# Optimization experiments

Hardware: AMD Instinct MI355X
Metric: run time of the kernel (lower is better)

Reference implementation:

```python
import jax, jax.numpy as jnp
import numpy as np

B, P, N, E = 4, 4, 4096, 512
QKV_DIM, HEADS = 512, 8
DH = QKV_DIM // HEADS
EPS = 1e-12  # F.normalize default eps


def setup_inputs() -> dict:
    key = jax.random.key(0)
    ks = jax.random.split(key, 5)
    s = 1.0 / np.sqrt(E)
    return {
        "x": jax.random.normal(ks[0], (B, P, N, E), dtype=jnp.float32),
        "w_qkv": jax.random.normal(ks[1], (3 * QKV_DIM, E), dtype=jnp.float32) * s,
        "b_qkv": jax.random.normal(ks[2], (3 * QKV_DIM,), dtype=jnp.float32) * 0.01,
        "temperature": jnp.ones((HEADS, 1, 1), dtype=jnp.float32),
        "w_out": jax.random.normal(ks[3], (E, QKV_DIM), dtype=jnp.float32) * (1.0 / np.sqrt(QKV_DIM)),
        "b_out": jax.random.normal(ks[4], (E,), dtype=jnp.float32) * 0.01,
    }


def _l2norm(t):
    # F.normalize(t, dim=-1): t / max(||t||_2, eps)
    n = jnp.sqrt(jnp.sum(t * t, axis=-1, keepdims=True))
    return t / jnp.maximum(n, EPS)


def reference(x, w_qkv, b_qkv, temperature, w_out, b_out):
    b, p, n, _ = x.shape
    qkv = x @ w_qkv.T + b_qkv                      # (b,p,n,3*qkv)
    q, k, v = jnp.split(qkv, 3, axis=-1)
    def to_heads(t):
        # (b,p,n,h*dh) -> (b,p,h,dh,n)  (channels-as-tokens)
        t = t.reshape(b, p, n, HEADS, DH)
        return jnp.transpose(t, (0, 1, 3, 4, 2))
    q, k, v = to_heads(q), to_heads(k), to_heads(v)
    q = _l2norm(q)                                  # normalize over tokens n
    k = _l2norm(k)
    # channel-wise (dh x dh) attention per head, temperature-scaled
    attn = jnp.einsum('bphdn,bphen->bphde', q, k) * temperature  # (b,p,h,dh,dh)
    attn = jax.nn.softmax(attn, axis=-1)
    out = jnp.einsum('bphde,bphen->bphdn', attn, v)               # (b,p,h,dh,n)
    # torch rearrange 'b p h n d -> b p d (h n)' on (b,p,h,dh,n) -> (b,p,n,h*dh)
    out = jnp.transpose(out, (0, 1, 4, 2, 3)).reshape(b, p, n, HEADS * DH)
    return out @ w_out.T + b_out
```

## Files before the change

### kernel.cpp

```cpp
#include <hip/hip_runtime.h>
#include <stdint.h>

typedef unsigned short u16;
typedef __bf16 bf16x8 __attribute__((ext_vector_type(8)));
typedef float f32x4 __attribute__((ext_vector_type(4)));

#define AS1 __attribute__((address_space(1)))
#define AS3 __attribute__((address_space(3)))

__device__ __forceinline__ void gload_lds16(u16* lds_wave_base, const u16* g) {
  __builtin_amdgcn_global_load_lds((AS1 void*)g, (AS3 void*)lds_wave_base, 16, 0, 0);
}

__device__ __forceinline__ u16 f2bf(float f) {
  unsigned int u = __float_as_uint(f);
  u += 0x7fffu + ((u >> 16) & 1u);
  return (u16)(u >> 16);
}

__global__ void cast_f32_bf16(const float* __restrict__ in, u16* __restrict__ out, int n8) {
  int i = blockIdx.x * blockDim.x + threadIdx.x;
  if (i >= n8) return;
  const float4* p = (const float4*)in + (size_t)i * 2;
  float4 a = p[0], b = p[1];
  uint2 lo, hi;
  lo.x = (unsigned)f2bf(a.x) | ((unsigned)f2bf(a.y) << 16);
  lo.y = (unsigned)f2bf(a.z) | ((unsigned)f2bf(a.w) << 16);
  hi.x = (unsigned)f2bf(b.x) | ((unsigned)f2bf(b.y) << 16);
  hi.y = (unsigned)f2bf(b.z) | ((unsigned)f2bf(b.w) << 16);
  uint2* o = (uint2*)out + (size_t)i * 2;
  o[0] = lo;
  o[1] = hi;
}

template <int MODE>
__global__ __launch_bounds__(256) void gemm_bt(const u16* __restrict__ gA,
                                               const u16* __restrict__ gB,
                                               const float* __restrict__ bias,
                                               void* __restrict__ gC,
                                               float* __restrict__ ssq) {
  constexpr int SMEM_U16 = (MODE == 2) ? 8192 : (128 * 136);
  __shared__ __align__(16) u16 smem[SMEM_U16];
  u16* As = smem;
  u16* Bs = smem + 4096;
  const int t = threadIdx.x;
  const int w = t >> 6, l = t & 63;
  const int lrow = l & 15, quad = l >> 4;
  const int wm = (w >> 1) * 64, wn = (w & 1) * 64;
  const int m0 = (MODE == 0 ? blockIdx.y : blockIdx.x) * 128;
  const int n0 = (MODE == 0 ? blockIdx.x : blockIdx.y) * 128;
  const u16* pA = gA;
  const u16* pB = gB;
  if (MODE == 2) {
    pA += (size_t)blockIdx.z * (512 * 512);
    pB += (size_t)blockIdx.z * (4096 * 512);
  }
  const int srow = w * 32 + (l >> 2);
  const int scol = (l & 3) * 8;
  const u16* ga0 = pA + (size_t)(m0 + srow) * 512 + scol;
  const u16* ga1 = pA + (size_t)(m0 + srow + 16) * 512 + scol;
  const u16* gb0 = pB + (size_t)(n0 + srow) * 512 + scol;
  const u16* gb1 = pB + (size_t)(n0 + srow + 16) * 512 + scol;
  u16* lA0 = &As[w * 1024];
  u16* lA1 = &As[w * 1024 + 512];
  u16* lB0 = &Bs[w * 1024];
  u16* lB1 = &Bs[w * 1024 + 512];

  f32x4 acc[4][4];
#pragma unroll
  for (int mi = 0; mi < 4; ++mi)
#pragma unroll
    for (int ni = 0; ni < 4; ++ni) acc[mi][ni] = (f32x4){0.f, 0.f, 0.f, 0.f};

#pragma unroll 1
  for (int k0 = 0; k0 < 512; k0 += 32) {
    gload_lds16(lA0, ga0 + k0);
    gload_lds16(lA1, ga1 + k0);
    gload_lds16(lB0, gb0 + k0);
    gload_lds16(lB1, gb1 + k0);
    __syncthreads();
    bf16x8 af[4], bfr[4];
#pragma unroll
    for (int mi = 0; mi < 4; ++mi)
      af[mi] = *(const bf16x8*)&As[(wm + mi * 16 + lrow) * 32 + quad * 8];
#pragma unroll
    for (int ni = 0; ni < 4; ++ni)
      bfr[ni] = *(const bf16x8*)&Bs[(wn + ni * 16 + lrow) * 32 + quad * 8];
#pragma unroll
    for (int mi = 0; mi < 4; ++mi)
#pragma unroll
      for (int ni = 0; ni < 4; ++ni)
        acc[mi][ni] = __builtin_amdgcn_mfma_f32_16x16x32_bf16(af[mi], bfr[ni], acc[mi][ni], 0, 0, 0);
    __syncthreads();
  }

  if (MODE == 2) {
#pragma unroll
    for (int mi = 0; mi < 4; ++mi) {
      const int mrow = m0 + wm + mi * 16 + quad * 4;
      const float4 bb = *(const float4*)&bias[mrow];
#pragma unroll
      for (int ni = 0; ni < 4; ++ni) {
        const int ncol = n0 + wn + ni * 16 + lrow;
        f32x4 v = acc[mi][ni];
        float4 o;
        o.x = v[0] + bb.x;
        o.y = v[1] + bb.y;
        o.z = v[2] + bb.z;
        o.w = v[3] + bb.w;
        *(float4*)((float*)gC + (((size_t)blockIdx.z * 4096 + ncol) * 512 + mrow)) = o;
      }
    }
  } else {
    float ss[4] = {0.f, 0.f, 0.f, 0.f};
#pragma unroll
    for (int mi = 0; mi < 4; ++mi) {
      const int mrow_l = wm + mi * 16 + quad * 4;
#pragma unroll
      for (int ni = 0; ni < 4; ++ni) {
        const int ncol_l = wn + ni * 16 + lrow;
        f32x4 v = acc[mi][ni];
        float f0, f1, f2, f3;
        if (MODE == 0) {
          const float bb = bias[n0 + ncol_l];
          f0 = v[0] + bb;
          f1 = v[1] + bb;
          f2 = v[2] + bb;
          f3 = v[3] + bb;
          ss[ni] += f0 * f0 + f1 * f1 + f2 * f2 + f3 * f3;
        } else {
          const float4 bb = *(const float4*)&bias[1024 + m0 + mrow_l];
          f0 = v[0] + bb.x;
          f1 = v[1] + bb.y;
          f2 = v[2] + bb.z;
          f3 = v[3] + bb.w;
        }
        uint2 pk;
        pk.x = (unsigned)f2bf(f0) | ((unsigned)f2bf(f1) << 16);
        pk.y = (unsigned)f2bf(f2) | ((unsigned)f2bf(f3) << 16);
        *(uint2*)&smem[ncol_l * 136 + mrow_l] = pk;
      }
    }
    if (MODE == 0) {
#pragma unroll
      for (int ni = 0; ni < 4; ++ni) {
        float s = ss[ni];
        s += __shfl_xor(s, 16);
        s += __shfl_xor(s, 32);
        if (quad == 0)
          atomicAdd(&ssq[((m0 >> 12) << 10) + n0 + wn + ni * 16 + lrow], s);
      }
    }
    __syncthreads();
    u16* outp = (u16*)gC;
#pragma unroll
    for (int j = 0; j < 8; ++j) {
      const int g = j * 256 + t;
      const int r = g >> 4;
      const int c = (g & 15) * 8;
      uint4 val = *(const uint4*)&smem[r * 136 + c];
      size_t gaddr;
      if (MODE == 0) {
        gaddr = ((size_t)(m0 >> 12) << 22) + ((size_t)(n0 + r) << 12) + (size_t)((m0 & 4095) + c);
      } else {
        const int tokg = n0 + r;
        gaddr = (size_t)(tokg >> 12) * (4096 * 512) + (size_t)(tokg & 4095) * 512 + (size_t)(m0 + c);
      }
      *(uint4*)(outp + gaddr) = val;
    }
  }
}

__global__ __launch_bounds__(512) void attn_weff(const u16* __restrict__ QKt,
                                                 const u16* __restrict__ wout,
                                                 const float* __restrict__ temperature,
                                                 const float* __restrict__ ssq,
                                                 u16* __restrict__ Weff) {
  __shared__ __align__(16) float sattn[64 * 64];
  __shared__ __align__(16) u16 sattnT[64 * 64];
  __shared__ float rn[128];
  const int blk = blockIdx.x;
  const int bp = blk >> 3, h = blk & 7;
  const int t = threadIdx.x, w = t >> 6, l = t & 63;
  const int lrow = l & 15, quad = l >> 4;
  const u16* base = QKt + ((size_t)bp << 22);

  for (int i = t; i < 4096; i += 512) sattn[i] = 0.f;

  if (t < 128) {
    const int ch = (t < 64) ? (h * 64 + t) : (448 + h * 64 + t);
    const float nn = sqrtf(ssq[(bp << 10) + ch]);
    rn[t] = 1.f / fmaxf(nn, 1e-12f);
  }

  f32x4 acc[4][4];
#pragma unroll
  for (int mi = 0; mi < 4; ++mi)
#pragma unroll
    for (int ni = 0; ni < 4; ++ni) acc[mi][ni] = (f32x4){0.f, 0.f, 0.f, 0.f};
  const u16* qb = base + ((size_t)(h * 64) << 12);
  const u16* kb = base + ((size_t)(512 + h * 64) << 12);
  const int nbase = w * 512;
#pragma unroll 1
  for (int ks = 0; ks < 16; ++ks) {
    const int nn = nbase + ks * 32 + quad * 8;
    bf16x8 af[4], bfr[4];
#pragma unroll
    for (int mi = 0; mi < 4; ++mi)
      af[mi] = *(const bf16x8*)(qb + (((size_t)(mi * 16 + lrow)) << 12) + nn);
#pragma unroll
    for (int ni = 0; ni < 4; ++ni)
      bfr[ni] = *(const bf16x8*)(kb + (((size_t)(ni * 16 + lrow)) << 12) + nn);
#pragma unroll
    for (int mi = 0; mi < 4; ++mi)
#pragma unroll
      for (int ni = 0; ni < 4; ++ni)
        acc[mi][ni] = __builtin_amdgcn_mfma_f32_16x16x32_bf16(af[mi], bfr[ni], acc[mi][ni], 0, 0, 0);
  }
  __syncthreads();
  for (int ww = 0; ww < 8; ++ww) {
    if (w == ww) {
#pragma unroll
      for (int mi = 0; mi < 4; ++mi)
#pragma unroll
        for (int ni = 0; ni < 4; ++ni)
#pragma unroll
          for (int r = 0; r < 4; ++r)
            sattn[(mi * 16 + quad * 4 + r) * 64 + ni * 16 + lrow] += acc[mi][ni][r];
    }
    __syncthreads();
  }

  if (t < 64) {
    const int d = t;
    const float rq = rn[d];
    const float tmp = temperature[h];
    float mx = -1e30f;
    for (int e = 0; e < 64; ++e) {
      const int idx = (e + d) & 63;
      float v = sattn[d * 64 + idx] * rq * rn[64 + idx] * tmp;
      sattn[d * 64 + idx] = v;
      mx = fmaxf(mx, v);
    }
    float s = 0.f;
    for (int e = 0; e < 64; ++e) {
      const int idx = (e + d) & 63;
      float p = __expf(sattn[d * 64 + idx] - mx);
      s += p;
      sattn[d * 64 + idx] = p;
    }
    const float inv = 1.f / s;
    for (int e = 0; e < 64; ++e) sattnT[e * 64 + d] = f2bf(sattn[d * 64 + e] * inv);
  }
  __syncthreads();

  bf16x8 a0[4], a1[4];
#pragma unroll
  for (int mi = 0; mi < 4; ++mi) {
    a0[mi] = *(const bf16x8*)&sattnT[(mi * 16 + lrow) * 64 + quad * 8];
    a1[mi] = *(const bf16x8*)&sattnT[(mi * 16 + lrow) * 64 + 32 + quad * 8];
  }
  u16* wb = Weff + ((size_t)bp * (512 * 512));
#pragma unroll 1
  for (int nb = 0; nb < 4; ++nb) {
    const int co = (w * 4 + nb) * 16 + lrow;
    const u16* wrow = wout + (size_t)co * 512 + h * 64;
    bf16x8 b0 = *(const bf16x8*)(wrow + quad * 8);
    bf16x8 b1 = *(const bf16x8*)(wrow + 32 + quad * 8);
#pragma unroll
    for (int mi = 0; mi < 4; ++mi) {
      f32x4 c = (f32x4){0.f, 0.f, 0.f, 0.f};
      c = __builtin_amdgcn_mfma_f32_16x16x32_bf16(a0[mi], b0, c, 0, 0, 0);
      c = __builtin_amdgcn_mfma_f32_16x16x32_bf16(a1[mi], b1, c, 0, 0, 0);
      const int e0 = mi * 16 + quad * 4;
      uint2 pk;
      pk.x = (unsigned)f2bf(c[0]) | ((unsigned)f2bf(c[1]) << 16);
      pk.y = (unsigned)f2bf(c[2]) | ((unsigned)f2bf(c[3]) << 16);
      *(uint2*)(wb + (size_t)co * 512 + h * 64 + e0) = pk;
    }
  }
}

extern "C" void kernel_launch(void* const* d_in, const int* in_sizes, int n_in,
                              void* d_out, int out_size, void* d_ws, size_t ws_size,
                              hipStream_t stream) {
  const float* x      = (const float*)d_in[0];
  const float* w_qkv  = (const float*)d_in[1];
  const float* b_qkv  = (const float*)d_in[2];
  const float* temp   = (const float*)d_in[3];
  const float* w_out  = (const float*)d_in[4];
  const float* b_out  = (const float*)d_in[5];
  float* y = (float*)d_out;

  char* ws = (char*)d_ws;
  u16* x_bf    = (u16*)(ws);
  u16* wqkv_bf = (u16*)(ws + 67108864);
  u16* wout_bf = (u16*)(ws + 68681728);
  u16* QKt     = (u16*)(ws + 69206016);
  u16* V_nat   = (u16*)(ws + 203423744);
  u16* Weff    = (u16*)(ws + 270532608);
  float* ssq   = (float*)(ws + 278921216);

  hipMemsetAsync(ssq, 0, 16 * 1024 * sizeof(float), stream);
  cast_f32_bf16<<<16384, 256, 0, stream>>>(x, x_bf, 33554432 / 8);
  cast_f32_bf16<<<384, 256, 0, stream>>>(w_qkv, wqkv_bf, 786432 / 8);
  cast_f32_bf16<<<128, 256, 0, stream>>>(w_out, wout_bf, 262144 / 8);

  gemm_bt<0><<<dim3(8, 512), 256, 0, stream>>>(x_bf, wqkv_bf, b_qkv, QKt, ssq);
  gemm_bt<1><<<dim3(4, 512), 256, 0, stream>>>(wqkv_bf + 1024 * 512, x_bf, b_qkv, V_nat, nullptr);
  attn_weff<<<128, 512, 0, stream>>>(QKt, wout_bf, temp, ssq, Weff);
  gemm_bt<2><<<dim3(4, 32, 16), 256, 0, stream>>>(Weff, V_nat, b_out, y, nullptr);
}
```

Measured before the change: 542.8 us.

## Split QK reduction across more blocks, swizzle GEMM tiles, stage output stores

The single attn_weff kernel, which launched only 128 blocks, becomes two kernels. A 1024-block qk_partial kernel computes per-chunk partial QK^T sums into workspace, and softmax_weff reduces the eight partials before doing the softmax and Weff. The GEMM grids are flattened and remapped so that groups of 8 consecutive blocks share input tiles, aiming for better L2 reuse. The final GEMM now stages its fp32 output through LDS to write coalesced row-major stores instead of scattered float4 writes. The cost is an extra launch and partial-sum traffic, plus a larger shared-memory footprint for MODE 2.

```diff
diff --git a/kernel.cpp b/kernel.cpp
--- a/kernel.cpp
+++ b/kernel.cpp
@@ -39,21 +39,40 @@
                                                const float* __restrict__ bias,
                                                void* __restrict__ gC,
                                                float* __restrict__ ssq) {
-  constexpr int SMEM_U16 = (MODE == 2) ? 8192 : (128 * 136);
-  __shared__ __align__(16) u16 smem[SMEM_U16];
+  __shared__ __align__(16) u16 smem[128 * 136];
   u16* As = smem;
   u16* Bs = smem + 4096;
   const int t = threadIdx.x;
   const int w = t >> 6, l = t & 63;
   const int lrow = l & 15, quad = l >> 4;
   const int wm = (w >> 1) * 64, wn = (w & 1) * 64;
-  const int m0 = (MODE == 0 ? blockIdx.y : blockIdx.x) * 128;
-  const int n0 = (MODE == 0 ? blockIdx.x : blockIdx.y) * 128;
+  int m0, n0, zz = 0;
+  if (MODE == 0) {
+    const int b = blockIdx.x;
+    const int ch = (b >> 3) & 7;
+    const int T = ((b >> 6) << 3) | (b & 7);
+    m0 = T * 128;
+    n0 = ch * 128;
+  } else if (MODE == 1) {
+    const int b = blockIdx.x;
+    const int j = (b >> 3) & 3;
+    const int T = ((b >> 5) << 3) | (b & 7);
+    m0 = j * 128;
+    n0 = T * 128;
+  } else {
+    const int b = blockIdx.x;
+    const int local = b & 127;
+    zz = b >> 7;
+    const int j = (local >> 3) & 3;
+    const int T = ((local >> 5) << 3) | (local & 7);
+    m0 = j * 128;
+    n0 = T * 128;
+  }
   const u16* pA = gA;
   const u16* pB = gB;
   if (MODE == 2) {
-    pA += (size_t)blockIdx.z * (512 * 512);
-    pB += (size_t)blockIdx.z * (4096 * 512);
+    pA += (size_t)zz * (512 * 512);
+    pB += (size_t)zz * (4096 * 512);
   }
   const int srow = w * 32 + (l >> 2);
   const int scol = (l & 3) * 8;
@@ -95,20 +114,38 @@
   }
 
   if (MODE == 2) {
-#pragma unroll
-    for (int mi = 0; mi < 4; ++mi) {
-      const int mrow = m0 + wm + mi * 16 + quad * 4;
-      const float4 bb = *(const float4*)&bias[mrow];
-#pragma unroll
-      for (int ni = 0; ni < 4; ++ni) {
-        const int ncol = n0 + wn + ni * 16 + lrow;
-        f32x4 v = acc[mi][ni];
-        float4 o;
-        o.x = v[0] + bb.x;
-        o.y = v[1] + bb.y;
-        o.z = v[2] + bb.z;
-        o.w = v[3] + bb.w;
-        *(float4*)((float*)gC + (((size_t)blockIdx.z * 4096 + ncol) * 512 + mrow)) = o;
+    float* fs = (float*)smem;
+#pragma unroll
+    for (int half = 0; half < 2; ++half) {
+      if (half) __syncthreads();
+#pragma unroll
+      for (int mi = 0; mi < 4; ++mi) {
+        const int mrow_l = wm + mi * 16 + quad * 4;
+        const float4 bb = *(const float4*)&bias[m0 + mrow_l];
+#pragma unroll
+        for (int ni = 0; ni < 4; ++ni) {
+          const int ncol_l = wn + ni * 16 + lrow;
+          if ((ncol_l >> 6) != half) continue;
+          f32x4 v = acc[mi][ni];
+          float4 o;
+          o.x = v[0] + bb.x;
+          o.y = v[1] + bb.y;
+          o.z = v[2] + bb.z;
+          o.w = v[3] + bb.w;
+          *(float4*)&fs[(ncol_l & 63) * 136 + mrow_l] = o;
+        }
+      }
+      __syncthreads();
+#pragma unroll
+      for (int j2 = 0; j2 < 4; ++j2) {
+        const int g = j2 * 256 + t;
+        const int r = g >> 4;
+        const int c = (g & 15) * 8;
+        float4 v0 = *(const float4*)&fs[r * 136 + c];
+        float4 v1 = *(const float4*)&fs[r * 136 + c + 4];
+        float* yp = (float*)gC + (((size_t)zz * 4096 + n0 + half * 64 + r) * 512 + m0 + c);
+        *(float4*)yp = v0;
+        *(float4*)(yp + 4) = v1;
       }
     }
   } else {
@@ -171,11 +208,67 @@
   }
 }
 
-__global__ __launch_bounds__(512) void attn_weff(const u16* __restrict__ QKt,
-                                                 const u16* __restrict__ wout,
-                                                 const float* __restrict__ temperature,
-                                                 const float* __restrict__ ssq,
-                                                 u16* __restrict__ Weff) {
+__global__ __launch_bounds__(256) void qk_partial(const u16* __restrict__ QKt,
+                                                  float* __restrict__ part) {
+  __shared__ __align__(16) float sred[64 * 64];
+  const int b = blockIdx.x;
+  const int chunk = b & 7, blk = b >> 3;
+  const int bp = blk >> 3, h = blk & 7;
+  const int t = threadIdx.x, w = t >> 6, l = t & 63;
+  const int lrow = l & 15, quad = l >> 4;
+  const u16* base = QKt + ((size_t)bp << 22);
+  const u16* qb = base + ((size_t)(h * 64) << 12);
+  const u16* kb = base + ((size_t)(512 + h * 64) << 12);
+  f32x4 acc[4][4];
+#pragma unroll
+  for (int mi = 0; mi < 4; ++mi)
+#pragma unroll
+    for (int ni = 0; ni < 4; ++ni) acc[mi][ni] = (f32x4){0.f, 0.f, 0.f, 0.f};
+  const int nbase = chunk * 512 + w * 128;
+#pragma unroll 1
+  for (int ks = 0; ks < 4; ++ks) {
+    const int nn = nbase + ks * 32 + quad * 8;
+    bf16x8 af[4], bfr[4];
+#pragma unroll
+    for (int mi = 0; mi < 4; ++mi)
+      af[mi] = *(const bf16x8*)(qb + (((size_t)(mi * 16 + lrow)) << 12) + nn);
+#pragma unroll
+    for (int ni = 0; ni < 4; ++ni)
+      bfr[ni] = *(const bf16x8*)(kb + (((size_t)(ni * 16 + lrow)) << 12) + nn);
+#pragma unroll
+    for (int mi = 0; mi < 4; ++mi)
+#pragma unroll
+      for (int ni = 0; ni < 4; ++ni)
+        acc[mi][ni] = __builtin_amdgcn_mfma_f32_16x16x32_bf16(af[mi], bfr[ni], acc[mi][ni], 0, 0, 0);
+  }
+  __syncthreads();
+  for (int ww = 0; ww < 4; ++ww) {
+    if (w == ww) {
+#pragma unroll
+      for (int mi = 0; mi < 4; ++mi)
+#pragma unroll
+        for (int ni = 0; ni < 4; ++ni)
+#pragma unroll
+          for (int r = 0; r < 4; ++r) {
+            const int idx = (mi * 16 + quad * 4 + r) * 64 + ni * 16 + lrow;
+            if (ww == 0)
+              sred[idx] = acc[mi][ni][r];
+            else
+              sred[idx] += acc[mi][ni][r];
+          }
+    }
+    __syncthreads();
+  }
+  float4* dst = (float4*)(part + ((size_t)blk * 8 + chunk) * 4096);
+  const float4* src = (const float4*)sred;
+  for (int i = t; i < 1024; i += 256) dst[i] = src[i];
+}
+
+__global__ __launch_bounds__(512) void softmax_weff(const float* __restrict__ part,
+                                                    const u16* __restrict__ wout,
+                                                    const float* __restrict__ temperature,
+                                                    const float* __restrict__ ssq,
+                                                    u16* __restrict__ Weff) {
   __shared__ __align__(16) float sattn[64 * 64];
   __shared__ __align__(16) u16 sattnT[64 * 64];
   __shared__ float rn[128];
@@ -183,53 +276,27 @@
   const int bp = blk >> 3, h = blk & 7;
   const int t = threadIdx.x, w = t >> 6, l = t & 63;
   const int lrow = l & 15, quad = l >> 4;
-  const u16* base = QKt + ((size_t)bp << 22);
-
-  for (int i = t; i < 4096; i += 512) sattn[i] = 0.f;
+
+  const float4* pbase = (const float4*)(part + (size_t)blk * 8 * 4096);
+  for (int i = t; i < 1024; i += 512) {
+    float4 s0 = pbase[i];
+#pragma unroll
+    for (int p = 1; p < 8; ++p) {
+      float4 sp = pbase[p * 1024 + i];
+      s0.x += sp.x;
+      s0.y += sp.y;
+      s0.z += sp.z;
+      s0.w += sp.w;
+    }
+    ((float4*)sattn)[i] = s0;
+  }
 
   if (t < 128) {
     const int ch = (t < 64) ? (h * 64 + t) : (448 + h * 64 + t);
     const float nn = sqrtf(ssq[(bp << 10) + ch]);
     rn[t] = 1.f / fmaxf(nn, 1e-12f);
   }
-
-  f32x4 acc[4][4];
-#pragma unroll
-  for (int mi = 0; mi < 4; ++mi)
-#pragma unroll
-    for (int ni = 0; ni < 4; ++ni) acc[mi][ni] = (f32x4){0.f, 0.f, 0.f, 0.f};
-  const u16* qb = base + ((size_t)(h * 64) << 12);
-  const u16* kb = base + ((size_t)(512 + h * 64) << 12);
-  const int nbase = w * 512;
-#pragma unroll 1
-  for (int ks = 0; ks < 16; ++ks) {
-    const int nn = nbase + ks * 32 + quad * 8;
-    bf16x8 af[4], bfr[4];
-#pragma unroll
-    for (int mi = 0; mi < 4; ++mi)
-      af[mi] = *(const bf16x8*)(qb + (((size_t)(mi * 16 + lrow)) << 12) + nn);
-#pragma unroll
-    for (int ni = 0; ni < 4; ++ni)
-      bfr[ni] = *(const bf16x8*)(kb + (((size_t)(ni * 16 + lrow)) << 12) + nn);
-#pragma unroll
-    for (int mi = 0; mi < 4; ++mi)
-#pragma unroll
-      for (int ni = 0; ni < 4; ++ni)
-        acc[mi][ni] = __builtin_amdgcn_mfma_f32_16x16x32_bf16(af[mi], bfr[ni], acc[mi][ni], 0, 0, 0);
-  }
   __syncthreads();
-  for (int ww = 0; ww < 8; ++ww) {
-    if (w == ww) {
-#pragma unroll
-      for (int mi = 0; mi < 4; ++mi)
-#pragma unroll
-        for (int ni = 0; ni < 4; ++ni)
-#pragma unroll
-          for (int r = 0; r < 4; ++r)
-            sattn[(mi * 16 + quad * 4 + r) * 64 + ni * 16 + lrow] += acc[mi][ni][r];
-    }
-    __syncthreads();
-  }
 
   if (t < 64) {
     const int d = t;
@@ -300,14 +367,16 @@
   u16* V_nat   = (u16*)(ws + 203423744);
   u16* Weff    = (u16*)(ws + 270532608);
   float* ssq   = (float*)(ws + 278921216);
+  float* part  = (float*)(ws);
 
   hipMemsetAsync(ssq, 0, 16 * 1024 * sizeof(float), stream);
   cast_f32_bf16<<<16384, 256, 0, stream>>>(x, x_bf, 33554432 / 8);
   cast_f32_bf16<<<384, 256, 0, stream>>>(w_qkv, wqkv_bf, 786432 / 8);
   cast_f32_bf16<<<128, 256, 0, stream>>>(w_out, wout_bf, 262144 / 8);
 
-  gemm_bt<0><<<dim3(8, 512), 256, 0, stream>>>(x_bf, wqkv_bf, b_qkv, QKt, ssq);
-  gemm_bt<1><<<dim3(4, 512), 256, 0, stream>>>(wqkv_bf + 1024 * 512, x_bf, b_qkv, V_nat, nullptr);
-  attn_weff<<<128, 512, 0, stream>>>(QKt, wout_bf, temp, ssq, Weff);
-  gemm_bt<2><<<dim3(4, 32, 16), 256, 0, stream>>>(Weff, V_nat, b_out, y, nullptr);
-}
+  gemm_bt<0><<<4096, 256, 0, stream>>>(x_bf, wqkv_bf, b_qkv, QKt, ssq);
+  gemm_bt<1><<<2048, 256, 0, stream>>>(wqkv_bf + 1024 * 512, x_bf, b_qkv, V_nat, nullptr);
+  qk_partial<<<1024, 256, 0, stream>>>(QKt, part);
+  softmax_weff<<<128, 512, 0, stream>>>(part, wout_bf, temp, ssq, Weff);
+  gemm_bt<2><<<2048, 256, 0, stream>>>(Weff, V_nat, b_out, y, nullptr);
+}
```

New measurement: 518.8 us. 1.05x faster.
